# Kernel tuning notes

Hardware: AMD Instinct MI355X
Metric: run time of the kernel (lower is better)

The kernel has to match this reference:

```python
import jax, jax.numpy as jnp
import numpy as np

EMBED_DIM = 8
THRESHOLD = 0.8
N_NODES = 8192
# QCNNModel (stack of FC layers mimicking quantum conv/pool steps):
# 8 -> 16 -> 16 -> 12 -> 8 -> 4 -> 1, tanh hidden activations, sigmoid head.
QCNN_DIMS = [8, 16, 16, 12, 8, 4, 1]


def setup_inputs() -> dict:
    key = jax.random.key(0)
    ks = jax.random.split(key, 20)
    inp = {
        "inputs": jax.random.normal(ks[0], (N_NODES, EMBED_DIM), dtype=jnp.float32),
        "rotation": jax.random.normal(ks[1], (EMBED_DIM, EMBED_DIM), dtype=jnp.float32),
        "entangle": jax.random.normal(ks[2], (EMBED_DIM, EMBED_DIM), dtype=jnp.float32),
        "gnn_w": jax.random.normal(ks[3], (EMBED_DIM, EMBED_DIM), dtype=jnp.float32) * 0.3,
        "gnn_b": jnp.zeros((EMBED_DIM,), dtype=jnp.float32),
    }
    for li in range(len(QCNN_DIMS) - 1):
        din, dout = QCNN_DIMS[li], QCNN_DIMS[li + 1]
        inp[f"qw{li}"] = jax.random.normal(ks[4 + 2 * li], (dout, din), dtype=jnp.float32) * (1.0 / np.sqrt(din))
        inp[f"qb{li}"] = jnp.zeros((dout,), dtype=jnp.float32)
    return inp


def _forward(inputs, rotation, entangle, gnn_w, gnn_b, qws, qbs):
    n = inputs.shape[0]
    # --- fidelity adjacency (vectorized Gram matrix + threshold) ---
    x = inputs / (jnp.linalg.norm(inputs, axis=1, keepdims=True) + 1e-12)
    fid = jnp.square(x @ x.T)                      # [n, n] |<i|j>|^2
    eye = jnp.eye(n, dtype=bool)
    adj = jnp.where((fid >= THRESHOLD) & ~eye, 1.0, 0.0).astype(inputs.dtype)
    # --- graph diffusion: neighbour sum + linear + relu ---
    neighbour_sum = adj @ inputs                   # [n, d]
    diffused = jax.nn.relu(neighbour_sum @ gnn_w.T + gnn_b)
    # --- self-attention (query=rotation, key=entangle, value=features) ---
    q = diffused @ rotation                        # [n, d]
    k = diffused @ entangle                        # [n, d]
    scores = jax.nn.softmax((q @ k.T) / jnp.sqrt(jnp.asarray(EMBED_DIM, inputs.dtype)), axis=-1)
    attended = scores @ diffused                   # [n, d]
    # --- QCNN fully-connected stack ---
    h = attended
    n_layers = len(qws)
    for li in range(n_layers):
        h = h @ qws[li].T + qbs[li]
        h = jax.nn.tanh(h) if li < n_layers - 1 else jax.nn.sigmoid(h)
    return h                                       # [n, 1]


def reference(inputs, rotation, entangle, gnn_w, gnn_b,
              qw0, qb0, qw1, qb1, qw2, qb2, qw3, qb3, qw4, qb4, qw5, qb5):
    qws = [qw0, qw1, qw2, qw3, qw4, qw5]
    qbs = [qb0, qb1, qb2, qb3, qb4, qb5]
    return _forward(inputs, rotation, entangle, gnn_w, gnn_b, qws, qbs)
```

## Files before the change

kernel.cpp:

```cpp
#include <hip/hip_runtime.h>
#include <math.h>

#define NN 8192

__device__ __forceinline__ float fexp2(float x) {
    float r;
    asm("v_exp_f32 %0, %1" : "=v"(r) : "v"(x));
    return r;
}

__global__ __launch_bounds__(256) void k_norm(const float* __restrict__ in,
                                              float* __restrict__ xn) {
    int r = blockIdx.x * 256 + threadIdx.x;
    const float4* p = reinterpret_cast<const float4*>(in + r * 8);
    float4 a = p[0], b = p[1];
    float ss = a.x*a.x + a.y*a.y + a.z*a.z + a.w*a.w
             + b.x*b.x + b.y*b.y + b.z*b.z + b.w*b.w;
    float inv = 1.0f / (sqrtf(ss) + 1e-12f);
    a.x *= inv; a.y *= inv; a.z *= inv; a.w *= inv;
    b.x *= inv; b.y *= inv; b.z *= inv; b.w *= inv;
    float4* o = reinterpret_cast<float4*>(xn + r * 8);
    o[0] = a; o[1] = b;
}

template<int SEGS, int IT>
__global__ __launch_bounds__(256) void k_adj_t(const float* __restrict__ xn,
                                               const float* __restrict__ in,
                                               float* __restrict__ pns) {
    constexpr int JC = NN / SEGS;
    constexpr int RSTR = NN / IT;
    __shared__ float4 sx[JC * 2];
    __shared__ float4 si[JC * 2];
    int tid = threadIdx.x;
    int r = blockIdx.x * 256 + tid;
    int seg = blockIdx.y;
    int j0 = seg * JC;

    for (int idx = tid; idx < JC * 2; idx += 256) {
        sx[idx] = reinterpret_cast<const float4*>(xn + (size_t)j0 * 8)[idx];
        si[idx] = reinterpret_cast<const float4*>(in + (size_t)j0 * 8)[idx];
    }
    float x[IT][8];
    #pragma unroll
    for (int i = 0; i < IT; ++i) {
        const float4* xp = reinterpret_cast<const float4*>(xn + (size_t)(r + i * RSTR) * 8);
        float4 a = xp[0], b = xp[1];
        x[i][0]=a.x; x[i][1]=a.y; x[i][2]=a.z; x[i][3]=a.w;
        x[i][4]=b.x; x[i][5]=b.y; x[i][6]=b.z; x[i][7]=b.w;
    }
    __syncthreads();

    float A[IT][8] = {};

    for (int c8 = 0; c8 < JC; c8 += 8) {
        #pragma unroll
        for (int u = 0; u < 8; ++u) {
            int t = c8 + u;
            int j = j0 + t;
            float4 a = sx[t * 2], b = sx[t * 2 + 1];
            bool hit[IT];
            bool hany = false;
            #pragma unroll
            for (int i = 0; i < IT; ++i) {
                float d = fmaf(x[i][7], b.w, fmaf(x[i][6], b.z,
                          fmaf(x[i][5], b.y, fmaf(x[i][4], b.x,
                          fmaf(x[i][3], a.w, fmaf(x[i][2], a.z,
                          fmaf(x[i][1], a.y, x[i][0] * a.x)))))));
                hit[i] = (d * d >= 0.8f) && (j != r + i * RSTR);
                hany = hany || hit[i];
            }
            if (hany) {
                float4 u0 = si[t * 2], u1 = si[t * 2 + 1];
                #pragma unroll
                for (int i = 0; i < IT; ++i) {
                    if (hit[i]) {
                        A[i][0]+=u0.x; A[i][1]+=u0.y; A[i][2]+=u0.z; A[i][3]+=u0.w;
                        A[i][4]+=u1.x; A[i][5]+=u1.y; A[i][6]+=u1.z; A[i][7]+=u1.w;
                    }
                }
            }
        }
    }
    #pragma unroll
    for (int i = 0; i < IT; ++i) {
        float4* o = reinterpret_cast<float4*>(pns + ((size_t)seg * NN + r + i * RSTR) * 8);
        o[0] = make_float4(A[i][0], A[i][1], A[i][2], A[i][3]);
        o[1] = make_float4(A[i][4], A[i][5], A[i][6], A[i][7]);
    }
}

__global__ __launch_bounds__(256) void k_diff2(const float* __restrict__ pns,
                                               const float* __restrict__ gw,
                                               const float* __restrict__ gb,
                                               const float* __restrict__ rot,
                                               const float* __restrict__ ent,
                                               float* __restrict__ dif,
                                               float* __restrict__ qsb,
                                               float* __restrict__ kkb,
                                               int nseg) {
    int tid = threadIdx.x;
    int sub = tid & 7;
    int row = blockIdx.x * 32 + (tid >> 3);
    float ns[8] = {0,0,0,0,0,0,0,0};
    for (int g = sub; g < nseg; g += 8) {
        const float4* p = reinterpret_cast<const float4*>(pns + ((size_t)g * NN + row) * 8);
        float4 a = p[0], b = p[1];
        ns[0]+=a.x; ns[1]+=a.y; ns[2]+=a.z; ns[3]+=a.w;
        ns[4]+=b.x; ns[5]+=b.y; ns[6]+=b.z; ns[7]+=b.w;
    }
    #pragma unroll
    for (int msk = 1; msk <= 4; msk <<= 1) {
        #pragma unroll
        for (int e = 0; e < 8; ++e) ns[e] += __shfl_xor(ns[e], msk);
    }
    if (sub == 0) {
        float df[8];
        #pragma unroll
        for (int d = 0; d < 8; ++d) {
            float v = gb[d];
            #pragma unroll
            for (int e = 0; e < 8; ++e) v += ns[e] * gw[d * 8 + e];
            df[d] = fmaxf(v, 0.0f);
        }
        const float QSC = (float)(1.4426950408889634 / 2.8284271247461903);
        #pragma unroll
        for (int d = 0; d < 8; ++d) {
            float vq = 0.0f, vk = 0.0f;
            #pragma unroll
            for (int e = 0; e < 8; ++e) {
                vq += df[e] * rot[e * 8 + d];
                vk += df[e] * ent[e * 8 + d];
            }
            qsb[row * 8 + d] = vq * QSC;
            kkb[row * 8 + d] = vk;
        }
        float4* o = reinterpret_cast<float4*>(dif + (size_t)row * 8);
        o[0] = make_float4(df[0], df[1], df[2], df[3]);
        o[1] = make_float4(df[4], df[5], df[6], df[7]);
    }
}

template<int SEGS, int IT>
__global__ __launch_bounds__(256) void k_attn_t(const float* __restrict__ qsb,
                                                const float* __restrict__ kkb,
                                                const float* __restrict__ dif,
                                                float* __restrict__ pacc,
                                                float* __restrict__ pm,
                                                float* __restrict__ psum) {
    constexpr int JC = NN / SEGS;
    constexpr int RSTR = NN / IT;
    __shared__ float4 sk[JC * 2];
    __shared__ float4 sd[JC * 2];
    int tid = threadIdx.x;
    int r = blockIdx.x * 256 + tid;
    int seg = blockIdx.y;
    int j0 = seg * JC;

    for (int idx = tid; idx < JC * 2; idx += 256) {
        sk[idx] = reinterpret_cast<const float4*>(kkb + (size_t)j0 * 8)[idx];
        sd[idx] = reinterpret_cast<const float4*>(dif + (size_t)j0 * 8)[idx];
    }
    float q[IT][8];
    #pragma unroll
    for (int i = 0; i < IT; ++i) {
        const float4* qp = reinterpret_cast<const float4*>(qsb + (size_t)(r + i * RSTR) * 8);
        float4 a = qp[0], b = qp[1];
        q[i][0]=a.x; q[i][1]=a.y; q[i][2]=a.z; q[i][3]=a.w;
        q[i][4]=b.x; q[i][5]=b.y; q[i][6]=b.z; q[i][7]=b.w;
    }
    __syncthreads();

    float m[IT], sum[IT];
    float A[IT][8] = {};
    #pragma unroll
    for (int i = 0; i < IT; ++i) { m[i] = -__builtin_huge_valf(); sum[i] = 0.0f; }

    for (int c8 = 0; c8 < JC; c8 += 8) {
        float s[IT][8];
        #pragma unroll
        for (int u = 0; u < 8; ++u) {
            int t = c8 + u;
            float4 ka = sk[t * 2], kb = sk[t * 2 + 1];
            #pragma unroll
            for (int i = 0; i < IT; ++i) {
                s[i][u] = fmaf(q[i][7], kb.w, fmaf(q[i][6], kb.z,
                          fmaf(q[i][5], kb.y, fmaf(q[i][4], kb.x,
                          fmaf(q[i][3], ka.w, fmaf(q[i][2], ka.z,
                          fmaf(q[i][1], ka.y, q[i][0] * ka.x)))))));
            }
        }
        #pragma unroll
        for (int i = 0; i < IT; ++i) {
            float cm = fmaxf(fmaxf(fmaxf(s[i][0], s[i][1]), fmaxf(s[i][2], s[i][3])),
                             fmaxf(fmaxf(s[i][4], s[i][5]), fmaxf(s[i][6], s[i][7])));
            float mn = fmaxf(m[i], cm);
            float rs = fexp2(m[i] - mn);
            m[i] = mn;
            sum[i] *= rs;
            #pragma unroll
            for (int e = 0; e < 8; ++e) A[i][e] *= rs;
        }
        #pragma unroll
        for (int u = 0; u < 8; ++u) {
            int t = c8 + u;
            float4 da = sd[t * 2], db = sd[t * 2 + 1];
            #pragma unroll
            for (int i = 0; i < IT; ++i) {
                float p = fexp2(s[i][u] - m[i]);
                sum[i] += p;
                A[i][0] = fmaf(p, da.x, A[i][0]); A[i][1] = fmaf(p, da.y, A[i][1]);
                A[i][2] = fmaf(p, da.z, A[i][2]); A[i][3] = fmaf(p, da.w, A[i][3]);
                A[i][4] = fmaf(p, db.x, A[i][4]); A[i][5] = fmaf(p, db.y, A[i][5]);
                A[i][6] = fmaf(p, db.z, A[i][6]); A[i][7] = fmaf(p, db.w, A[i][7]);
            }
        }
    }

    #pragma unroll
    for (int i = 0; i < IT; ++i) {
        size_t b = (size_t)seg * NN + r + i * RSTR;
        float4* o = reinterpret_cast<float4*>(pacc + b * 8);
        o[0] = make_float4(A[i][0], A[i][1], A[i][2], A[i][3]);
        o[1] = make_float4(A[i][4], A[i][5], A[i][6], A[i][7]);
        pm[b] = m[i];
        psum[b] = sum[i];
    }
}

__global__ __launch_bounds__(256) void k_merge2(const float* __restrict__ pacc,
                                                const float* __restrict__ pm,
                                                const float* __restrict__ psum,
                                                const float* __restrict__ qw0, const float* __restrict__ qb0,
                                                const float* __restrict__ qw1, const float* __restrict__ qb1,
                                                const float* __restrict__ qw2, const float* __restrict__ qb2,
                                                const float* __restrict__ qw3, const float* __restrict__ qb3,
                                                const float* __restrict__ qw4, const float* __restrict__ qb4,
                                                const float* __restrict__ qw5, const float* __restrict__ qb5,
                                                float* __restrict__ out,
                                                int nseg) {
    int tid = threadIdx.x;
    int sub = tid & 7;
    int row = blockIdx.x * 32 + (tid >> 3);

    float m = -3.0e38f, T = 0.0f;
    float A[8] = {0,0,0,0,0,0,0,0};
    for (int g = sub; g < nseg; g += 8) {
        size_t base = (size_t)g * NN + row;
        float mg = pm[base];
        float newm = fmaxf(m, mg);
        float cs = fexp2(m - newm);
        float cg = fexp2(mg - newm);
        T = fmaf(T, cs, psum[base] * cg);
        const float4* p = reinterpret_cast<const float4*>(pacc + base * 8);
        float4 a = p[0], b = p[1];
        A[0] = fmaf(A[0], cs, a.x * cg); A[1] = fmaf(A[1], cs, a.y * cg);
        A[2] = fmaf(A[2], cs, a.z * cg); A[3] = fmaf(A[3], cs, a.w * cg);
        A[4] = fmaf(A[4], cs, b.x * cg); A[5] = fmaf(A[5], cs, b.y * cg);
        A[6] = fmaf(A[6], cs, b.z * cg); A[7] = fmaf(A[7], cs, b.w * cg);
        m = newm;
    }
    #pragma unroll
    for (int msk = 1; msk <= 4; msk <<= 1) {
        float mo = __shfl_xor(m, msk);
        float To = __shfl_xor(T, msk);
        float Ao[8];
        #pragma unroll
        for (int e = 0; e < 8; ++e) Ao[e] = __shfl_xor(A[e], msk);
        float newm = fmaxf(m, mo);
        float cs = fexp2(m - newm);
        float co = fexp2(mo - newm);
        T = T * cs + To * co;
        #pragma unroll
        for (int e = 0; e < 8; ++e) A[e] = A[e] * cs + Ao[e] * co;
        m = newm;
    }

    if (sub == 0) {
        float invT = 1.0f / T;
        float h0[8];
        #pragma unroll
        for (int d = 0; d < 8; ++d) h0[d] = A[d] * invT;

        float h1[16];
        #pragma unroll
        for (int t = 0; t < 16; ++t) {
            float v = qb0[t];
            #pragma unroll
            for (int e = 0; e < 8; ++e) v += h0[e] * qw0[t * 8 + e];
            h1[t] = tanhf(v);
        }
        float h2[16];
        #pragma unroll
        for (int t = 0; t < 16; ++t) {
            float v = qb1[t];
            #pragma unroll
            for (int e = 0; e < 16; ++e) v += h1[e] * qw1[t * 16 + e];
            h2[t] = tanhf(v);
        }
        float h3[12];
        #pragma unroll
        for (int t = 0; t < 12; ++t) {
            float v = qb2[t];
            #pragma unroll
            for (int e = 0; e < 16; ++e) v += h2[e] * qw2[t * 16 + e];
            h3[t] = tanhf(v);
        }
        float h4[8];
        #pragma unroll
        for (int t = 0; t < 8; ++t) {
            float v = qb3[t];
            #pragma unroll
            for (int e = 0; e < 12; ++e) v += h3[e] * qw3[t * 12 + e];
            h4[t] = tanhf(v);
        }
        float h5[4];
        #pragma unroll
        for (int t = 0; t < 4; ++t) {
            float v = qb4[t];
            #pragma unroll
            for (int e = 0; e < 8; ++e) v += h4[e] * qw4[t * 8 + e];
            h5[t] = tanhf(v);
        }
        float o = qb5[0];
        #pragma unroll
        for (int e = 0; e < 4; ++e) o += h5[e] * qw5[e];
        out[row] = 1.0f / (1.0f + expf(-o));
    }
}

extern "C" void kernel_launch(void* const* d_in, const int* in_sizes, int n_in,
                              void* d_out, int out_size, void* d_ws, size_t ws_size,
                              hipStream_t stream) {
    const float* in  = (const float*)d_in[0];
    const float* rot = (const float*)d_in[1];
    const float* ent = (const float*)d_in[2];
    const float* gw  = (const float*)d_in[3];
    const float* gb  = (const float*)d_in[4];
    const float* qw0 = (const float*)d_in[5];
    const float* qb0 = (const float*)d_in[6];
    const float* qw1 = (const float*)d_in[7];
    const float* qb1 = (const float*)d_in[8];
    const float* qw2 = (const float*)d_in[9];
    const float* qb2 = (const float*)d_in[10];
    const float* qw3 = (const float*)d_in[11];
    const float* qb3 = (const float*)d_in[12];
    const float* qw4 = (const float*)d_in[13];
    const float* qb4 = (const float*)d_in[14];
    const float* qw5 = (const float*)d_in[15];
    const float* qb5 = (const float*)d_in[16];

    auto need = [](int nseg) { return ((size_t)NN * 8 * 4 + (size_t)nseg * NN * 18) * 4; };
    int nseg;
    if (ws_size >= need(128)) nseg = 128;
    else if (ws_size >= need(64)) nseg = 64;
    else nseg = 32;

    float* ws = (float*)d_ws;
    size_t off = 0;
    float* xn   = ws + off; off += (size_t)NN * 8;
    float* pns  = ws + off; off += (size_t)nseg * NN * 8;
    float* dif  = ws + off; off += (size_t)NN * 8;
    float* qsb  = ws + off; off += (size_t)NN * 8;
    float* kkb  = ws + off; off += (size_t)NN * 8;
    float* pacc = ws + off; off += (size_t)nseg * NN * 8;
    float* pm   = ws + off; off += (size_t)nseg * NN;
    float* psum = ws + off; off += (size_t)nseg * NN;

    dim3 blk(256);
    k_norm<<<dim3(NN / 256), blk, 0, stream>>>(in, xn);
    if (nseg == 128) {
        k_adj_t<128, 4><<<dim3(NN / 4 / 256, 128), blk, 0, stream>>>(xn, in, pns);
    } else if (nseg == 64) {
        k_adj_t<64, 4><<<dim3(NN / 4 / 256, 64), blk, 0, stream>>>(xn, in, pns);
    } else {
        k_adj_t<32, 2><<<dim3(NN / 2 / 256, 32), blk, 0, stream>>>(xn, in, pns);
    }
    k_diff2<<<dim3(NN / 32), blk, 0, stream>>>(pns, gw, gb, rot, ent, dif, qsb, kkb, nseg);
    if (nseg == 128) {
        k_attn_t<128, 4><<<dim3(NN / 4 / 256, 128), blk, 0, stream>>>(qsb, kkb, dif, pacc, pm, psum);
    } else if (nseg == 64) {
        k_attn_t<64, 4><<<dim3(NN / 4 / 256, 64), blk, 0, stream>>>(qsb, kkb, dif, pacc, pm, psum);
    } else {
        k_attn_t<32, 2><<<dim3(NN / 2 / 256, 32), blk, 0, stream>>>(qsb, kkb, dif, pacc, pm, psum);
    }
    k_merge2<<<dim3(NN / 32), blk, 0, stream>>>(pacc, pm, psum,
                                                qw0, qb0, qw1, qb1, qw2, qb2,
                                                qw3, qb3, qw4, qb4, qw5, qb5,
                                                (float*)d_out, nseg);
}
```

Measured before the change: 116.9 us.

## Replace LDS-tiled adj/attn kernels with lane-split column-major global streaming

Adds transposed copies of normalized inputs, raw inputs, keys and diffused features. The adjacency and attention kernels are rewritten so that 8 lanes share one row and stride over columns read directly from global memory, with shuffle reductions at the end. The number of column segments is fixed at 4 instead of being chosen from workspace size. This removes the LDS staging, the syncs and the large partial buffers. In exchange it drops multi-row register reuse per thread and adds per-iteration global loads and a branchy online softmax.

```diff
diff --git a/kernel.cpp b/kernel.cpp
--- a/kernel.cpp
+++ b/kernel.cpp
@@ -2,6 +2,7 @@
 #include <math.h>
 
 #define NN 8192
+#define SA 4
 
 __device__ __forceinline__ float fexp2(float x) {
     float r;
@@ -10,82 +11,72 @@
 }
 
 __global__ __launch_bounds__(256) void k_norm(const float* __restrict__ in,
-                                              float* __restrict__ xn) {
+                                              float* __restrict__ xn,
+                                              float* __restrict__ xnT,
+                                              float* __restrict__ inT) {
     int r = blockIdx.x * 256 + threadIdx.x;
-    const float4* p = reinterpret_cast<const float4*>(in + r * 8);
+    const float4* p = reinterpret_cast<const float4*>(in + (size_t)r * 8);
     float4 a = p[0], b = p[1];
+    float raw[8] = {a.x, a.y, a.z, a.w, b.x, b.y, b.z, b.w};
     float ss = a.x*a.x + a.y*a.y + a.z*a.z + a.w*a.w
              + b.x*b.x + b.y*b.y + b.z*b.z + b.w*b.w;
     float inv = 1.0f / (sqrtf(ss) + 1e-12f);
-    a.x *= inv; a.y *= inv; a.z *= inv; a.w *= inv;
-    b.x *= inv; b.y *= inv; b.z *= inv; b.w *= inv;
-    float4* o = reinterpret_cast<float4*>(xn + r * 8);
-    o[0] = a; o[1] = b;
-}
-
-template<int SEGS, int IT>
-__global__ __launch_bounds__(256) void k_adj_t(const float* __restrict__ xn,
-                                               const float* __restrict__ in,
-                                               float* __restrict__ pns) {
-    constexpr int JC = NN / SEGS;
-    constexpr int RSTR = NN / IT;
-    __shared__ float4 sx[JC * 2];
-    __shared__ float4 si[JC * 2];
+    float nv[8];
+    #pragma unroll
+    for (int e = 0; e < 8; ++e) nv[e] = raw[e] * inv;
+    float4* o = reinterpret_cast<float4*>(xn + (size_t)r * 8);
+    o[0] = make_float4(nv[0], nv[1], nv[2], nv[3]);
+    o[1] = make_float4(nv[4], nv[5], nv[6], nv[7]);
+    #pragma unroll
+    for (int e = 0; e < 8; ++e) {
+        xnT[(size_t)e * NN + r] = nv[e];
+        inT[(size_t)e * NN + r] = raw[e];
+    }
+}
+
+__global__ __launch_bounds__(256) void k_adj3(const float* __restrict__ xn,
+                                              const float* __restrict__ xnT,
+                                              const float* __restrict__ inT,
+                                              float* __restrict__ pns) {
     int tid = threadIdx.x;
-    int r = blockIdx.x * 256 + tid;
+    int lane = tid & 63;
+    int w = tid >> 6;
+    int rt = blockIdx.x * 4 + w;
+    int r = rt * 8 + (lane >> 3);
     int seg = blockIdx.y;
-    int j0 = seg * JC;
-
-    for (int idx = tid; idx < JC * 2; idx += 256) {
-        sx[idx] = reinterpret_cast<const float4*>(xn + (size_t)j0 * 8)[idx];
-        si[idx] = reinterpret_cast<const float4*>(in + (size_t)j0 * 8)[idx];
-    }
-    float x[IT][8];
-    #pragma unroll
-    for (int i = 0; i < IT; ++i) {
-        const float4* xp = reinterpret_cast<const float4*>(xn + (size_t)(r + i * RSTR) * 8);
-        float4 a = xp[0], b = xp[1];
-        x[i][0]=a.x; x[i][1]=a.y; x[i][2]=a.z; x[i][3]=a.w;
-        x[i][4]=b.x; x[i][5]=b.y; x[i][6]=b.z; x[i][7]=b.w;
-    }
-    __syncthreads();
-
-    float A[IT][8] = {};
-
-    for (int c8 = 0; c8 < JC; c8 += 8) {
-        #pragma unroll
-        for (int u = 0; u < 8; ++u) {
-            int t = c8 + u;
-            int j = j0 + t;
-            float4 a = sx[t * 2], b = sx[t * 2 + 1];
-            bool hit[IT];
-            bool hany = false;
-            #pragma unroll
-            for (int i = 0; i < IT; ++i) {
-                float d = fmaf(x[i][7], b.w, fmaf(x[i][6], b.z,
-                          fmaf(x[i][5], b.y, fmaf(x[i][4], b.x,
-                          fmaf(x[i][3], a.w, fmaf(x[i][2], a.z,
-                          fmaf(x[i][1], a.y, x[i][0] * a.x)))))));
-                hit[i] = (d * d >= 0.8f) && (j != r + i * RSTR);
-                hany = hany || hit[i];
-            }
-            if (hany) {
-                float4 u0 = si[t * 2], u1 = si[t * 2 + 1];
-                #pragma unroll
-                for (int i = 0; i < IT; ++i) {
-                    if (hit[i]) {
-                        A[i][0]+=u0.x; A[i][1]+=u0.y; A[i][2]+=u0.z; A[i][3]+=u0.w;
-                        A[i][4]+=u1.x; A[i][5]+=u1.y; A[i][6]+=u1.z; A[i][7]+=u1.w;
-                    }
-                }
-            }
-        }
-    }
-    #pragma unroll
-    for (int i = 0; i < IT; ++i) {
-        float4* o = reinterpret_cast<float4*>(pns + ((size_t)seg * NN + r + i * RSTR) * 8);
-        o[0] = make_float4(A[i][0], A[i][1], A[i][2], A[i][3]);
-        o[1] = make_float4(A[i][4], A[i][5], A[i][6], A[i][7]);
+    const int JPW = NN / SA;
+    int j0 = seg * JPW;
+
+    float x[8];
+    #pragma unroll
+    for (int e = 0; e < 8; ++e) x[e] = xn[(size_t)r * 8 + e];
+
+    float A[8] = {0,0,0,0,0,0,0,0};
+
+    #pragma unroll 2
+    for (int t = 0; t < JPW / 8; ++t) {
+        int j = j0 + t * 8 + (lane & 7);
+        float xv[8];
+        #pragma unroll
+        for (int e = 0; e < 8; ++e) xv[e] = xnT[(size_t)e * NN + j];
+        float d = fmaf(x[7], xv[7], fmaf(x[6], xv[6],
+                  fmaf(x[5], xv[5], fmaf(x[4], xv[4],
+                  fmaf(x[3], xv[3], fmaf(x[2], xv[2],
+                  fmaf(x[1], xv[1], x[0] * xv[0])))))));
+        if (d * d >= 0.8f && j != r) {
+            #pragma unroll
+            for (int e = 0; e < 8; ++e) A[e] += inT[(size_t)e * NN + j];
+        }
+    }
+    #pragma unroll
+    for (int msk = 1; msk <= 4; msk <<= 1) {
+        #pragma unroll
+        for (int e = 0; e < 8; ++e) A[e] += __shfl_xor(A[e], msk);
+    }
+    if ((lane & 7) == 0) {
+        float4* o = reinterpret_cast<float4*>(pns + ((size_t)seg * NN + r) * 8);
+        o[0] = make_float4(A[0], A[1], A[2], A[3]);
+        o[1] = make_float4(A[4], A[5], A[6], A[7]);
     }
 }
 
@@ -94,15 +85,14 @@
                                                const float* __restrict__ gb,
                                                const float* __restrict__ rot,
                                                const float* __restrict__ ent,
-                                               float* __restrict__ dif,
+                                               float* __restrict__ difT,
                                                float* __restrict__ qsb,
-                                               float* __restrict__ kkb,
-                                               int nseg) {
+                                               float* __restrict__ kT) {
     int tid = threadIdx.x;
     int sub = tid & 7;
     int row = blockIdx.x * 32 + (tid >> 3);
     float ns[8] = {0,0,0,0,0,0,0,0};
-    for (int g = sub; g < nseg; g += 8) {
+    for (int g = sub; g < SA; g += 8) {
         const float4* p = reinterpret_cast<const float4*>(pns + ((size_t)g * NN + row) * 8);
         float4 a = p[0], b = p[1];
         ns[0]+=a.x; ns[1]+=a.y; ns[2]+=a.z; ns[3]+=a.w;
@@ -131,99 +121,82 @@
                 vq += df[e] * rot[e * 8 + d];
                 vk += df[e] * ent[e * 8 + d];
             }
-            qsb[row * 8 + d] = vq * QSC;
-            kkb[row * 8 + d] = vk;
-        }
-        float4* o = reinterpret_cast<float4*>(dif + (size_t)row * 8);
-        o[0] = make_float4(df[0], df[1], df[2], df[3]);
-        o[1] = make_float4(df[4], df[5], df[6], df[7]);
-    }
-}
-
-template<int SEGS, int IT>
-__global__ __launch_bounds__(256) void k_attn_t(const float* __restrict__ qsb,
-                                                const float* __restrict__ kkb,
-                                                const float* __restrict__ dif,
-                                                float* __restrict__ pacc,
-                                                float* __restrict__ pm,
-                                                float* __restrict__ psum) {
-    constexpr int JC = NN / SEGS;
-    constexpr int RSTR = NN / IT;
-    __shared__ float4 sk[JC * 2];
-    __shared__ float4 sd[JC * 2];
+            qsb[(size_t)row * 8 + d] = vq * QSC;
+            kT[(size_t)d * NN + row] = vk;
+            difT[(size_t)d * NN + row] = df[d];
+        }
+    }
+}
+
+__global__ __launch_bounds__(256) void k_attn3(const float* __restrict__ qsb,
+                                               const float* __restrict__ kT,
+                                               const float* __restrict__ difT,
+                                               float* __restrict__ pacc,
+                                               float* __restrict__ pm,
+                                               float* __restrict__ psum) {
     int tid = threadIdx.x;
-    int r = blockIdx.x * 256 + tid;
+    int lane = tid & 63;
+    int w = tid >> 6;
+    int rt = blockIdx.x * 4 + w;
+    int r = rt * 8 + (lane >> 3);
     int seg = blockIdx.y;
-    int j0 = seg * JC;
-
-    for (int idx = tid; idx < JC * 2; idx += 256) {
-        sk[idx] = reinterpret_cast<const float4*>(kkb + (size_t)j0 * 8)[idx];
-        sd[idx] = reinterpret_cast<const float4*>(dif + (size_t)j0 * 8)[idx];
-    }
-    float q[IT][8];
-    #pragma unroll
-    for (int i = 0; i < IT; ++i) {
-        const float4* qp = reinterpret_cast<const float4*>(qsb + (size_t)(r + i * RSTR) * 8);
-        float4 a = qp[0], b = qp[1];
-        q[i][0]=a.x; q[i][1]=a.y; q[i][2]=a.z; q[i][3]=a.w;
-        q[i][4]=b.x; q[i][5]=b.y; q[i][6]=b.z; q[i][7]=b.w;
-    }
-    __syncthreads();
-
-    float m[IT], sum[IT];
-    float A[IT][8] = {};
-    #pragma unroll
-    for (int i = 0; i < IT; ++i) { m[i] = -__builtin_huge_valf(); sum[i] = 0.0f; }
-
-    for (int c8 = 0; c8 < JC; c8 += 8) {
-        float s[IT][8];
-        #pragma unroll
-        for (int u = 0; u < 8; ++u) {
-            int t = c8 + u;
-            float4 ka = sk[t * 2], kb = sk[t * 2 + 1];
-            #pragma unroll
-            for (int i = 0; i < IT; ++i) {
-                s[i][u] = fmaf(q[i][7], kb.w, fmaf(q[i][6], kb.z,
-                          fmaf(q[i][5], kb.y, fmaf(q[i][4], kb.x,
-                          fmaf(q[i][3], ka.w, fmaf(q[i][2], ka.z,
-                          fmaf(q[i][1], ka.y, q[i][0] * ka.x)))))));
-            }
-        }
-        #pragma unroll
-        for (int i = 0; i < IT; ++i) {
-            float cm = fmaxf(fmaxf(fmaxf(s[i][0], s[i][1]), fmaxf(s[i][2], s[i][3])),
-                             fmaxf(fmaxf(s[i][4], s[i][5]), fmaxf(s[i][6], s[i][7])));
-            float mn = fmaxf(m[i], cm);
-            float rs = fexp2(m[i] - mn);
-            m[i] = mn;
-            sum[i] *= rs;
-            #pragma unroll
-            for (int e = 0; e < 8; ++e) A[i][e] *= rs;
-        }
-        #pragma unroll
-        for (int u = 0; u < 8; ++u) {
-            int t = c8 + u;
-            float4 da = sd[t * 2], db = sd[t * 2 + 1];
-            #pragma unroll
-            for (int i = 0; i < IT; ++i) {
-                float p = fexp2(s[i][u] - m[i]);
-                sum[i] += p;
-                A[i][0] = fmaf(p, da.x, A[i][0]); A[i][1] = fmaf(p, da.y, A[i][1]);
-                A[i][2] = fmaf(p, da.z, A[i][2]); A[i][3] = fmaf(p, da.w, A[i][3]);
-                A[i][4] = fmaf(p, db.x, A[i][4]); A[i][5] = fmaf(p, db.y, A[i][5]);
-                A[i][6] = fmaf(p, db.z, A[i][6]); A[i][7] = fmaf(p, db.w, A[i][7]);
-            }
-        }
-    }
-
-    #pragma unroll
-    for (int i = 0; i < IT; ++i) {
-        size_t b = (size_t)seg * NN + r + i * RSTR;
+    const int JPW = NN / SA;
+    int j0 = seg * JPW;
+
+    float q[8];
+    #pragma unroll
+    for (int e = 0; e < 8; ++e) q[e] = qsb[(size_t)r * 8 + e];
+
+    float m = -3.0e38f, sum = 0.0f;
+    float A[8] = {0,0,0,0,0,0,0,0};
+
+    #pragma unroll 2
+    for (int t = 0; t < JPW / 8; ++t) {
+        int j = j0 + t * 8 + (lane & 7);
+        float kv[8], dv[8];
+        #pragma unroll
+        for (int e = 0; e < 8; ++e) kv[e] = kT[(size_t)e * NN + j];
+        #pragma unroll
+        for (int e = 0; e < 8; ++e) dv[e] = difT[(size_t)e * NN + j];
+        float s = fmaf(q[7], kv[7], fmaf(q[6], kv[6],
+                  fmaf(q[5], kv[5], fmaf(q[4], kv[4],
+                  fmaf(q[3], kv[3], fmaf(q[2], kv[2],
+                  fmaf(q[1], kv[1], q[0] * kv[0])))))));
+        if (s > m) {
+            float c = fexp2(m - s);
+            m = s;
+            sum = fmaf(sum, c, 1.0f);
+            #pragma unroll
+            for (int e = 0; e < 8; ++e) A[e] = fmaf(A[e], c, dv[e]);
+        } else {
+            float p = fexp2(s - m);
+            sum += p;
+            #pragma unroll
+            for (int e = 0; e < 8; ++e) A[e] = fmaf(p, dv[e], A[e]);
+        }
+    }
+    #pragma unroll
+    for (int msk = 1; msk <= 4; msk <<= 1) {
+        float mo = __shfl_xor(m, msk);
+        float To = __shfl_xor(sum, msk);
+        float Ao[8];
+        #pragma unroll
+        for (int e = 0; e < 8; ++e) Ao[e] = __shfl_xor(A[e], msk);
+        float newm = fmaxf(m, mo);
+        float cs = fexp2(m - newm);
+        float co = fexp2(mo - newm);
+        sum = sum * cs + To * co;
+        #pragma unroll
+        for (int e = 0; e < 8; ++e) A[e] = A[e] * cs + Ao[e] * co;
+        m = newm;
+    }
+    if ((lane & 7) == 0) {
+        size_t b = (size_t)seg * NN + r;
         float4* o = reinterpret_cast<float4*>(pacc + b * 8);
-        o[0] = make_float4(A[i][0], A[i][1], A[i][2], A[i][3]);
-        o[1] = make_float4(A[i][4], A[i][5], A[i][6], A[i][7]);
-        pm[b] = m[i];
-        psum[b] = sum[i];
+        o[0] = make_float4(A[0], A[1], A[2], A[3]);
+        o[1] = make_float4(A[4], A[5], A[6], A[7]);
+        pm[b] = m;
+        psum[b] = sum;
     }
 }
 
@@ -236,15 +209,14 @@
                                                 const float* __restrict__ qw3, const float* __restrict__ qb3,
                                                 const float* __restrict__ qw4, const float* __restrict__ qb4,
                                                 const float* __restrict__ qw5, const float* __restrict__ qb5,
-                                                float* __restrict__ out,
-                                                int nseg) {
+                                                float* __restrict__ out) {
     int tid = threadIdx.x;
     int sub = tid & 7;
     int row = blockIdx.x * 32 + (tid >> 3);
 
     float m = -3.0e38f, T = 0.0f;
     float A[8] = {0,0,0,0,0,0,0,0};
-    for (int g = sub; g < nseg; g += 8) {
+    for (int g = sub; g < SA; g += 8) {
         size_t base = (size_t)g * NN + row;
         float mg = pm[base];
         float newm = fmaxf(m, mg);
@@ -349,42 +321,26 @@
     const float* qw5 = (const float*)d_in[15];
     const float* qb5 = (const float*)d_in[16];
 
-    auto need = [](int nseg) { return ((size_t)NN * 8 * 4 + (size_t)nseg * NN * 18) * 4; };
-    int nseg;
-    if (ws_size >= need(128)) nseg = 128;
-    else if (ws_size >= need(64)) nseg = 64;
-    else nseg = 32;
-
     float* ws = (float*)d_ws;
     size_t off = 0;
     float* xn   = ws + off; off += (size_t)NN * 8;
-    float* pns  = ws + off; off += (size_t)nseg * NN * 8;
-    float* dif  = ws + off; off += (size_t)NN * 8;
+    float* xnT  = ws + off; off += (size_t)NN * 8;
+    float* inT  = ws + off; off += (size_t)NN * 8;
+    float* pns  = ws + off; off += (size_t)SA * NN * 8;
     float* qsb  = ws + off; off += (size_t)NN * 8;
-    float* kkb  = ws + off; off += (size_t)NN * 8;
-    float* pacc = ws + off; off += (size_t)nseg * NN * 8;
-    float* pm   = ws + off; off += (size_t)nseg * NN;
-    float* psum = ws + off; off += (size_t)nseg * NN;
+    float* kT   = ws + off; off += (size_t)NN * 8;
+    float* difT = ws + off; off += (size_t)NN * 8;
+    float* pacc = ws + off; off += (size_t)SA * NN * 8;
+    float* pm   = ws + off; off += (size_t)SA * NN;
+    float* psum = ws + off; off += (size_t)SA * NN;
 
     dim3 blk(256);
-    k_norm<<<dim3(NN / 256), blk, 0, stream>>>(in, xn);
-    if (nseg == 128) {
-        k_adj_t<128, 4><<<dim3(NN / 4 / 256, 128), blk, 0, stream>>>(xn, in, pns);
-    } else if (nseg == 64) {
-        k_adj_t<64, 4><<<dim3(NN / 4 / 256, 64), blk, 0, stream>>>(xn, in, pns);
-    } else {
-        k_adj_t<32, 2><<<dim3(NN / 2 / 256, 32), blk, 0, stream>>>(xn, in, pns);
-    }
-    k_diff2<<<dim3(NN / 32), blk, 0, stream>>>(pns, gw, gb, rot, ent, dif, qsb, kkb, nseg);
-    if (nseg == 128) {
-        k_attn_t<128, 4><<<dim3(NN / 4 / 256, 128), blk, 0, stream>>>(qsb, kkb, dif, pacc, pm, psum);
-    } else if (nseg == 64) {
-        k_attn_t<64, 4><<<dim3(NN / 4 / 256, 64), blk, 0, stream>>>(qsb, kkb, dif, pacc, pm, psum);
-    } else {
-        k_attn_t<32, 2><<<dim3(NN / 2 / 256, 32), blk, 0, stream>>>(qsb, kkb, dif, pacc, pm, psum);
-    }
+    k_norm<<<dim3(NN / 256), blk, 0, stream>>>(in, xn, xnT, inT);
+    k_adj3<<<dim3(NN / 8 / 4, SA), blk, 0, stream>>>(xn, xnT, inT, pns);
+    k_diff2<<<dim3(NN / 32), blk, 0, stream>>>(pns, gw, gb, rot, ent, difT, qsb, kT);
+    k_attn3<<<dim3(NN / 8 / 4, SA), blk, 0, stream>>>(qsb, kT, difT, pacc, pm, psum);
     k_merge2<<<dim3(NN / 32), blk, 0, stream>>>(pacc, pm, psum,
                                                 qw0, qb0, qw1, qb1, qw2, qb2,
                                                 qw3, qb3, qw4, qb4, qw5, qb5,
-                                                (float*)d_out, nseg);
-}
+                                                (float*)d_out);
+}
```

Result: slower. 252.3 us (+115.9%).
